# Kernel tuning notes

Hardware: AMD Instinct MI355X
Metric: run time of the kernel (lower is better)

The kernel has to match this reference:

```python
import jax, jax.numpy as jnp
import numpy as np
from jax import lax

P = 10  # patch_size


def _conv(x, w, b, pad):
    y = lax.conv_general_dilated(x, w, (1, 1), [(pad, pad), (pad, pad)],
                                 dimension_numbers=('NCHW', 'OIHW', 'NCHW'))
    return y + b[None, :, None, None]


def setup_inputs() -> dict:
    key = jax.random.key(0)
    ks = jax.random.split(key, 9)
    B, Cin, H, W = 8, 3, 320, 320
    classes = 2
    p2 = P * P
    s = 0.05
    return {
        'x': jax.random.normal(ks[0], (B, Cin, H, W), jnp.float32),
        'w_conv1': jax.random.normal(ks[1], (64, Cin, 7, 7), jnp.float32) * s,
        'b_conv1': jax.random.normal(ks[2], (64,), jnp.float32) * s,
        'w_conv2': jax.random.normal(ks[3], (classes, 64, 3, 3), jnp.float32) * s,
        'b_conv2': jax.random.normal(ks[4], (classes,), jnp.float32) * s,
        'w_fm': jax.random.normal(ks[5], (classes, Cin, 1, 1), jnp.float32) * s,
        'b_fm': jax.random.normal(ks[6], (classes,), jnp.float32) * s,
        'w_lin1': jax.random.normal(ks[7], (2 * p2, p2), jnp.float32) * s,  # torch Linear [out,in]
        'w_lin2': jax.random.normal(ks[8], (p2, 2 * p2), jnp.float32) * s,
    }


def reference(x, w_conv1, b_conv1, w_conv2, b_conv2, w_fm, b_fm, w_lin1, w_lin2):
    p = P
    ini = _conv(_conv(x, w_conv1, b_conv1, 3), w_conv2, b_conv2, 1)  # [B,classes,H,W]
    fea = _conv(x, w_fm, b_fm, 0) / 4.0                              # [B,classes,H,W]
    B, C, H, W = ini.shape
    L = (H // p) * (W // p)

    def unfold(t):  # non-overlapping patches: [B,C,H,W] -> [B,C,L,p*p]
        t = t.reshape(B, C, H // p, p, W // p, p)
        return t.transpose(0, 1, 2, 4, 3, 5).reshape(B, C, L, p * p)

    def trans(t):  # Linear(p2->2p2) -> Linear(2p2->p2) -> ReLU, per patch
        h = jnp.einsum('bclp,qp->bclq', t, w_lin1)
        return jax.nn.relu(jnp.einsum('bclq,pq->bclp', h, w_lin2))

    ui = trans(unfold(ini))   # [B,C,L,p2]
    uf = trans(unfold(fea))   # [B,C,L,p2]
    att = jnp.einsum('bclp,bcmp->bclm', ui, uf) / (p * p)  # [B,C,L,L]
    return att
```

## Files before the change

### kernel.cpp

```cpp
#include <hip/hip_runtime.h>

#define WS_M      0
#define WS_K      10000
#define WS_BETA   12646
#define WS_W9     12664
#define WS_BT     13150
#define WS_UIT    (16384 + 1638400)
#define WS_UFT    (16384 + 2*1638400)

typedef short bf16x8 __attribute__((ext_vector_type(8)));
typedef float f32x4  __attribute__((ext_vector_type(4)));

__device__ inline ushort f2bf(float f) {
    unsigned u = __float_as_uint(f);
    unsigned r = (u + 0x7fffu + ((u >> 16) & 1u)) >> 16;
    return (ushort)r;
}

__global__ __launch_bounds__(256) void k_prep(const float* __restrict__ wl1,
                                              const float* __restrict__ wl2,
                                              const float* __restrict__ wc1,
                                              const float* __restrict__ bc1,
                                              const float* __restrict__ wc2,
                                              const float* __restrict__ bc2,
                                              float* __restrict__ ws) {
    int blk = blockIdx.x;
    int t = threadIdx.x;
    if (blk < 40) {
        int idx = blk * 256 + t;
        if (idx < 10000) {
            int p = idx / 100, r = idx % 100;
            float s = 0.f;
            for (int q = 0; q < 200; ++q)
                s += wl2[p * 200 + q] * wl1[q * 100 + r];
            ws[WS_M + r * 100 + p] = s;
        }
        return;
    }
    __shared__ float swc1[9408];
    __shared__ float swc2[1152];
    __shared__ float sBeta[18];
    for (int i = t; i < 9408; i += 256) swc1[i] = wc1[i];
    for (int i = t; i < 1152; i += 256) swc2[i] = wc2[i];
    __syncthreads();
    if (blk < 43) {
        int base = (blk - 40) * 882;
        for (int ii = t; ii < 882; ii += 256) {
            int idx = base + ii;
            int v = idx % 7; int t1 = idx / 7;
            int u = t1 % 7;  int t2 = t1 / 7;
            int ci = t2 % 3; int t3 = t2 / 3;
            int b = t3 % 3;  int t4 = t3 / 3;
            int a = t4 % 3;  int c = t4 / 3;
            float s = 0.f;
            for (int c64 = 0; c64 < 64; ++c64)
                s += swc2[((c * 64 + c64) * 3 + a) * 3 + b] *
                     swc1[((c64 * 3 + ci) * 7 + u) * 7 + v];
            ws[WS_K + idx] = s;
        }
        if (blk == 40) {
            if (t < 18) {
                int b = t % 3; int a = (t / 3) % 3; int c = t / 9;
                float s = 0.f;
                for (int c64 = 0; c64 < 64; ++c64)
                    s += swc2[((c * 64 + c64) * 3 + a) * 3 + b] * bc1[c64];
                sBeta[t] = s; ws[WS_BETA + t] = s;
            }
            __syncthreads();
            if (t < 2) {
                float s = bc2[t];
                for (int j2 = 0; j2 < 9; ++j2) s += sBeta[t * 9 + j2];
                ws[WS_BT + t] = s;
            }
        }
    } else {
        int idx = (blk - 43) * 243 + t;
        if (t < 243) {
            int dx = idx % 9; int t1 = idx / 9;
            int dy = t1 % 9;  int t2 = t1 / 9;
            int ci = t2 % 3;  int c = t2 / 3;
            float s = 0.f;
            for (int a = 0; a < 3; ++a) {
                int u = dy - a; if (u < 0 || u > 6) continue;
                for (int b = 0; b < 3; ++b) {
                    int v = dx - b; if (v < 0 || v > 6) continue;
                    for (int c64 = 0; c64 < 64; ++c64)
                        s += swc2[((c * 64 + c64) * 3 + a) * 3 + b] *
                             swc1[((c64 * 3 + ci) * 7 + u) * 7 + v];
                }
            }
            ws[WS_W9 + idx] = s;
        }
    }
}

__global__ __launch_bounds__(256, 8) void k_fuse(const float* __restrict__ x,
                                                 const float* __restrict__ wfm,
                                                 const float* __restrict__ bfm,
                                                 const float* __restrict__ ws,
                                                 ushort* __restrict__ uiL,
                                                 ushort* __restrict__ ufL) {
    union alignas(16) SMemU {
        float  sx[3][28][36];
        ushort sOut[2][2][4][128];
    };
    __shared__ SMemU smu;
    __shared__ float sP[2][2][100][4];
    const int bx = blockIdx.x, by = blockIdx.y, b = blockIdx.z;
    const int t = threadIdx.x;
    const float* Mt   = ws + WS_M;
    const float* Kw   = ws + WS_K;
    const float* Beta = ws + WS_BETA;
    const float* W9   = ws + WS_W9;
    const float* Bt   = ws + WS_BT;
    const int gh0 = by * 20, gw0 = bx * 20;
    bool edgeblk = (by == 0) | (by == 15) | (bx == 0) | (bx == 15);

    if (!edgeblk) {
        for (int i = t; i < 588; i += 256) {
            int ci = i / 196; int rem = i - ci * 196;
            int rr = rem / 7, c4 = rem - rr * 7;
            float4 v = *(const float4*)&x[(b * 3 + ci) * 102400 +
                                          (gh0 - 4 + rr) * 320 + (gw0 - 4) + c4 * 4];
            *(float4*)&smu.sx[ci][rr][c4 * 4] = v;
        }
    } else {
        for (int idx = t; idx < 3 * 28 * 28; idx += 256) {
            int ci = idx / 784; int rem = idx - ci * 784;
            int rr = rem / 28, cc = rem - rr * 28;
            int gh = gh0 - 4 + rr, gw = gw0 - 4 + cc;
            float v = 0.f;
            if ((unsigned)gh < 320u && (unsigned)gw < 320u)
                v = x[(b * 3 + ci) * 102400 + gh * 320 + gw];
            smu.sx[ci][rr][cc] = v;
        }
    }
    __syncthreads();

    const int lh = t / 10, lw0 = (t % 10) * 2;
    if (t < 200) {
        float acc0[2], acc1[2];
        float bt0 = Bt[0], bt1 = Bt[1];
        acc0[0] = bt0; acc0[1] = bt0; acc1[0] = bt1; acc1[1] = bt1;
        #pragma unroll
        for (int ci = 0; ci < 3; ++ci) {
            #pragma unroll
            for (int dy = 0; dy < 9; ++dy) {
                const float* xr = &smu.sx[ci][lh + dy][lw0];
                float2 y0 = *(const float2*)(xr);
                float2 y1 = *(const float2*)(xr + 2);
                float2 y2 = *(const float2*)(xr + 4);
                float2 y3 = *(const float2*)(xr + 6);
                float2 y4 = *(const float2*)(xr + 8);
                float xv[10] = {y0.x, y0.y, y1.x, y1.y, y2.x,
                                y2.y, y3.x, y3.y, y4.x, y4.y};
                #pragma unroll
                for (int dx = 0; dx < 9; ++dx) {
                    float w0t = W9[ci * 81 + dy * 9 + dx];
                    float w1t = W9[243 + ci * 81 + dy * 9 + dx];
                    acc0[0] += w0t * xv[dx];
                    acc0[1] += w0t * xv[dx + 1];
                    acc1[0] += w1t * xv[dx];
                    acc1[1] += w1t * xv[dx + 1];
                }
            }
        }
        if (edgeblk) {
            #pragma unroll
            for (int j = 0; j < 2; ++j) {
                int h = gh0 + lh, w = gw0 + lw0 + j;
                if (h == 0 || h == 319 || w == 0 || w == 319) {
                    float c0 = 0.f, c1 = 0.f;
                    for (int a = 0; a < 3; ++a) {
                        int hh = h + a - 1;
                        for (int bb = 0; bb < 3; ++bb) {
                            int wwp = w + bb - 1;
                            bool invalid = ((unsigned)hh >= 320u) |
                                           ((unsigned)wwp >= 320u);
                            if (invalid) {
                                c0 += Beta[a * 3 + bb];
                                c1 += Beta[9 + a * 3 + bb];
                                for (int ci = 0; ci < 3; ++ci) {
                                    const float* Kc = Kw + ((a * 3 + bb) * 3 + ci) * 49;
                                    #pragma unroll
                                    for (int u = 0; u < 7; ++u) {
                                        #pragma unroll
                                        for (int v = 0; v < 7; ++v) {
                                            float xv = smu.sx[ci][lh + a + u][lw0 + j + bb + v];
                                            c0 += Kc[u * 7 + v] * xv;
                                            c1 += Kc[1323 + u * 7 + v] * xv;
                                        }
                                    }
                                }
                            }
                        }
                    }
                    acc0[j] -= c0;
                    acc1[j] -= c1;
                }
            }
        }
        float wf00 = wfm[0], wf01 = wfm[1], wf02 = wfm[2];
        float wf10 = wfm[3], wf11 = wfm[4], wf12 = wfm[5];
        float bf0 = bfm[0], bf1 = bfm[1];
        #pragma unroll
        for (int j = 0; j < 2; ++j) {
            int lw = lw0 + j;
            int li = (lh / 10) * 2 + lw / 10;
            int r  = (lh % 10) * 10 + lw % 10;
            sP[0][0][r][li] = acc0[j];
            sP[0][1][r][li] = acc1[j];
            float s0 = smu.sx[0][4 + lh][4 + lw];
            float s1 = smu.sx[1][4 + lh][4 + lw];
            float s2 = smu.sx[2][4 + lh][4 + lw];
            sP[1][0][r][li] = (bf0 + s0 * wf00 + s1 * wf01 + s2 * wf02) * 0.25f;
            sP[1][1][r][li] = (bf1 + s0 * wf10 + s1 * wf11 + s2 * wf12) * 0.25f;
        }
    }
    __syncthreads();

    if (t < 200) {
        int plane = (t >= 100) ? 1 : 0;
        int p = t - plane * 100;
        float ai[4] = {0.f, 0.f, 0.f, 0.f};
        float af[4] = {0.f, 0.f, 0.f, 0.f};
        #pragma unroll 4
        for (int r = 0; r < 100; ++r) {
            float m = Mt[r * 100 + p];
            f32x4 si = *(const f32x4*)&sP[0][plane][r][0];
            f32x4 sf = *(const f32x4*)&sP[1][plane][r][0];
            #pragma unroll
            for (int k = 0; k < 4; ++k) {
                ai[k] += m * si[k];
                af[k] += m * sf[k];
            }
        }
        #pragma unroll
        for (int k = 0; k < 4; ++k) {
            smu.sOut[0][plane][k][p] = f2bf(fmaxf(ai[k], 0.f));
            smu.sOut[1][plane][k][p] = f2bf(fmaxf(af[k], 0.f));
        }
    } else {
        #pragma unroll
        for (int pass = 0; pass < 2; ++pass) {
            int task = (t - 200) + pass * 56;
            int mat = task / 56; int rem = task % 56;
            int plane = rem / 28; int rem2 = rem % 28;
            int k = rem2 / 7, q = rem2 % 7;
            *(uint2*)&smu.sOut[mat][plane][k][100 + q * 4] = make_uint2(0u, 0u);
        }
    }
    __syncthreads();

    {
        int mat = t >> 7;
        int row = (t >> 4) & 7;
        int plane = row >> 2, k = row & 3;
        int lane16 = t & 15;
        int bc = b * 2 + plane;
        int l = (by * 2 + (k >> 1)) * 32 + bx * 2 + (k & 1);
        ushort* dst = mat ? ufL : uiL;
        uint4 v = *(const uint4*)&smu.sOut[mat][plane][k][lane16 * 8];
        *(uint4*)&dst[((size_t)bc * 1024 + l) * 128 + lane16 * 8] = v;
    }
}

__global__ __launch_bounds__(256) void k_att(const ushort* __restrict__ ui,
                                             const ushort* __restrict__ uf,
                                             float* __restrict__ out) {
    int bc   = blockIdx.z;
    int row0 = blockIdx.y * 64, col0 = blockIdx.x * 128;
    int wave = threadIdx.x >> 6, lane = threadIdx.x & 63;
    int r0 = row0 + (wave >> 1) * 32;
    int c0 = col0 + (wave & 1) * 64;
    int m = lane & 15, quad = lane >> 4;
    const ushort* ub = ui + (size_t)bc * 1024 * 128;
    const ushort* vb = uf + (size_t)bc * 1024 * 128;
    f32x4 acc[2][4];
    #pragma unroll
    for (int i = 0; i < 2; ++i)
        #pragma unroll
        for (int j = 0; j < 4; ++j)
            acc[i][j] = (f32x4){0.f, 0.f, 0.f, 0.f};
    #pragma unroll
    for (int k0 = 0; k0 < 128; k0 += 32) {
        bf16x8 af[2], bfr[4];
        #pragma unroll
        for (int i = 0; i < 2; ++i)
            af[i] = *(const bf16x8*)&ub[(size_t)(r0 + i * 16 + m) * 128 + k0 + quad * 8];
        #pragma unroll
        for (int j = 0; j < 4; ++j)
            bfr[j] = *(const bf16x8*)&vb[(size_t)(c0 + j * 16 + m) * 128 + k0 + quad * 8];
        #pragma unroll
        for (int i = 0; i < 2; ++i)
            #pragma unroll
            for (int j = 0; j < 4; ++j)
                acc[i][j] = __builtin_amdgcn_mfma_f32_16x16x32_bf16(af[i], bfr[j], acc[i][j], 0, 0, 0);
    }
    #pragma unroll
    for (int i = 0; i < 2; ++i) {
        #pragma unroll
        for (int r = 0; r < 4; ++r) {
            int row = r0 + i * 16 + quad * 4 + r;
            float* o = out + ((size_t)bc * 1024 + row) * 1024;
            #pragma unroll
            for (int j = 0; j < 4; ++j)
                o[c0 + j * 16 + m] = acc[i][j][r] * 0.01f;
        }
    }
}

extern "C" void kernel_launch(void* const* d_in, const int* in_sizes, int n_in,
                              void* d_out, int out_size, void* d_ws, size_t ws_size,
                              hipStream_t stream) {
    const float* x       = (const float*)d_in[0];
    const float* w_conv1 = (const float*)d_in[1];
    const float* b_conv1 = (const float*)d_in[2];
    const float* w_conv2 = (const float*)d_in[3];
    const float* b_conv2 = (const float*)d_in[4];
    const float* w_fm    = (const float*)d_in[5];
    const float* b_fm    = (const float*)d_in[6];
    const float* w_lin1  = (const float*)d_in[7];
    const float* w_lin2  = (const float*)d_in[8];
    float* out = (float*)d_out;
    float* ws  = (float*)d_ws;
    ushort* uiL = (ushort*)(ws + WS_UIT);
    ushort* ufL = (ushort*)(ws + WS_UFT);

    k_prep<<<45, 256, 0, stream>>>(w_lin1, w_lin2, w_conv1, b_conv1, w_conv2, b_conv2, ws);
    k_fuse<<<dim3(16, 16, 8), 256, 0, stream>>>(x, w_fm, b_fm, ws, uiL, ufL);
    k_att<<<dim3(8, 16, 16), 256, 0, stream>>>(uiL, ufL, out);
}
```

Before: 201.3 us.

## Split fused conv+patch-transform kernel into separate conv and transform kernels

```diff
diff --git a/kernel.cpp b/kernel.cpp
--- a/kernel.cpp
+++ b/kernel.cpp
@@ -5,6 +5,7 @@
 #define WS_BETA   12646
 #define WS_W9     12664
 #define WS_BT     13150
+#define WS_INI    16384
 #define WS_UIT    (16384 + 1638400)
 #define WS_UFT    (16384 + 2*1638400)
 
@@ -94,21 +95,12 @@
     }
 }
 
-__global__ __launch_bounds__(256, 8) void k_fuse(const float* __restrict__ x,
-                                                 const float* __restrict__ wfm,
-                                                 const float* __restrict__ bfm,
+__global__ __launch_bounds__(256, 8) void k_conv(const float* __restrict__ x,
                                                  const float* __restrict__ ws,
-                                                 ushort* __restrict__ uiL,
-                                                 ushort* __restrict__ ufL) {
-    union alignas(16) SMemU {
-        float  sx[3][28][36];
-        ushort sOut[2][2][4][128];
-    };
-    __shared__ SMemU smu;
-    __shared__ float sP[2][2][100][4];
+                                                 float* __restrict__ ini) {
+    __shared__ float sx[3][28][36];
     const int bx = blockIdx.x, by = blockIdx.y, b = blockIdx.z;
     const int t = threadIdx.x;
-    const float* Mt   = ws + WS_M;
     const float* Kw   = ws + WS_K;
     const float* Beta = ws + WS_BETA;
     const float* W9   = ws + WS_W9;
@@ -122,7 +114,7 @@
             int rr = rem / 7, c4 = rem - rr * 7;
             float4 v = *(const float4*)&x[(b * 3 + ci) * 102400 +
                                           (gh0 - 4 + rr) * 320 + (gw0 - 4) + c4 * 4];
-            *(float4*)&smu.sx[ci][rr][c4 * 4] = v;
+            *(float4*)&sx[ci][rr][c4 * 4] = v;
         }
     } else {
         for (int idx = t; idx < 3 * 28 * 28; idx += 256) {
@@ -132,7 +124,7 @@
             float v = 0.f;
             if ((unsigned)gh < 320u && (unsigned)gw < 320u)
                 v = x[(b * 3 + ci) * 102400 + gh * 320 + gw];
-            smu.sx[ci][rr][cc] = v;
+            sx[ci][rr][cc] = v;
         }
     }
     __syncthreads();
@@ -146,7 +138,7 @@
         for (int ci = 0; ci < 3; ++ci) {
             #pragma unroll
             for (int dy = 0; dy < 9; ++dy) {
-                const float* xr = &smu.sx[ci][lh + dy][lw0];
+                const float* xr = &sx[ci][lh + dy][lw0];
                 float2 y0 = *(const float2*)(xr);
                 float2 y1 = *(const float2*)(xr + 2);
                 float2 y2 = *(const float2*)(xr + 4);
@@ -186,7 +178,7 @@
                                     for (int u = 0; u < 7; ++u) {
                                         #pragma unroll
                                         for (int v = 0; v < 7; ++v) {
-                                            float xv = smu.sx[ci][lh + a + u][lw0 + j + bb + v];
+                                            float xv = sx[ci][lh + a + u][lw0 + j + bb + v];
                                             c0 += Kc[u * 7 + v] * xv;
                                             c1 += Kc[1323 + u * 7 + v] * xv;
                                         }
@@ -200,68 +192,106 @@
                 }
             }
         }
-        float wf00 = wfm[0], wf01 = wfm[1], wf02 = wfm[2];
-        float wf10 = wfm[3], wf11 = wfm[4], wf12 = wfm[5];
-        float bf0 = bfm[0], bf1 = bfm[1];
-        #pragma unroll
-        for (int j = 0; j < 2; ++j) {
-            int lw = lw0 + j;
-            int li = (lh / 10) * 2 + lw / 10;
-            int r  = (lh % 10) * 10 + lw % 10;
-            sP[0][0][r][li] = acc0[j];
-            sP[0][1][r][li] = acc1[j];
-            float s0 = smu.sx[0][4 + lh][4 + lw];
-            float s1 = smu.sx[1][4 + lh][4 + lw];
-            float s2 = smu.sx[2][4 + lh][4 + lw];
-            sP[1][0][r][li] = (bf0 + s0 * wf00 + s1 * wf01 + s2 * wf02) * 0.25f;
-            sP[1][1][r][li] = (bf1 + s0 * wf10 + s1 * wf11 + s2 * wf12) * 0.25f;
+        size_t obase = (size_t)(b * 2) * 102400 + (gh0 + lh) * 320 + gw0 + lw0;
+        *(float2*)&ini[obase] = make_float2(acc0[0], acc0[1]);
+        *(float2*)&ini[obase + 102400] = make_float2(acc1[0], acc1[1]);
+    }
+}
+
+__global__ __launch_bounds__(256) void k_trans(const float* __restrict__ ini,
+                                               const float* __restrict__ x,
+                                               const float* __restrict__ wfm,
+                                               const float* __restrict__ bfm,
+                                               const float* __restrict__ ws,
+                                               ushort* __restrict__ uiL,
+                                               ushort* __restrict__ ufL) {
+    __shared__ float  sP[100][68];
+    __shared__ ushort sOut[64][64];
+    int bc = blockIdx.x;
+    int lg = blockIdx.y;
+    int zz = blockIdx.z;
+    int mode = zz >> 1, pg = zz & 1;
+    ushort* outL = mode ? ufL : uiL;
+    int t = threadIdx.x;
+    const float* Mt = ws + WS_M;
+    int b = bc >> 1, c = bc & 1;
+    int row0 = lg * 20;
+
+    if (mode == 0) {
+        for (int e = t; e < 1600; e += 256) {
+            int irow = e / 80, c4 = (e % 80) * 4;
+            float4 v = *(const float4*)&ini[bc * 102400 + (row0 + irow) * 320 + c4];
+            float vv[4] = {v.x, v.y, v.z, v.w};
+            #pragma unroll
+            for (int k = 0; k < 4; ++k) {
+                int col = c4 + k;
+                sP[(irow % 10) * 10 + col % 10][(irow / 10) * 32 + col / 10] = vv[k];
+            }
+        }
+    } else {
+        float wf0 = wfm[c * 3 + 0], wf1 = wfm[c * 3 + 1], wf2 = wfm[c * 3 + 2];
+        float bfv = bfm[c];
+        for (int e = t; e < 1600; e += 256) {
+            int irow = e / 80, c4 = (e % 80) * 4;
+            size_t base = (size_t)b * 3 * 102400 + (row0 + irow) * 320 + c4;
+            float4 v0 = *(const float4*)&x[base];
+            float4 v1 = *(const float4*)&x[base + 102400];
+            float4 v2 = *(const float4*)&x[base + 204800];
+            float a0[4] = {v0.x, v0.y, v0.z, v0.w};
+            float a1[4] = {v1.x, v1.y, v1.z, v1.w};
+            float a2[4] = {v2.x, v2.y, v2.z, v2.w};
+            #pragma unroll
+            for (int k = 0; k < 4; ++k) {
+                int col = c4 + k;
+                float val = (bfv + a0[k] * wf0 + a1[k] * wf1 + a2[k] * wf2) * 0.25f;
+                sP[(irow % 10) * 10 + col % 10][(irow / 10) * 32 + col / 10] = val;
+            }
         }
     }
     __syncthreads();
 
     if (t < 200) {
-        int plane = (t >= 100) ? 1 : 0;
-        int p = t - plane * 100;
-        float ai[4] = {0.f, 0.f, 0.f, 0.f};
-        float af[4] = {0.f, 0.f, 0.f, 0.f};
-        #pragma unroll 4
+        int py = t / 8, lx = t % 8;
+        int p0 = py * 2, lo = lx * 8;
+        float acc[2][8];
+        #pragma unroll
+        for (int i = 0; i < 2; ++i)
+            #pragma unroll
+            for (int j = 0; j < 8; ++j) acc[i][j] = 0.f;
+        #pragma unroll 5
         for (int r = 0; r < 100; ++r) {
-            float m = Mt[r * 100 + p];
-            f32x4 si = *(const f32x4*)&sP[0][plane][r][0];
-            f32x4 sf = *(const f32x4*)&sP[1][plane][r][0];
-            #pragma unroll
-            for (int k = 0; k < 4; ++k) {
-                ai[k] += m * si[k];
-                af[k] += m * sf[k];
-            }
-        }
-        #pragma unroll
-        for (int k = 0; k < 4; ++k) {
-            smu.sOut[0][plane][k][p] = f2bf(fmaxf(ai[k], 0.f));
-            smu.sOut[1][plane][k][p] = f2bf(fmaxf(af[k], 0.f));
+            float2 mv = *(const float2*)&Mt[r * 100 + pg * 50 + p0];
+            f32x4 b0 = *(const f32x4*)&sP[r][lo];
+            f32x4 b1 = *(const f32x4*)&sP[r][lo + 4];
+            #pragma unroll
+            for (int j = 0; j < 4; ++j) {
+                acc[0][j]     += mv.x * b0[j];
+                acc[0][4 + j] += mv.x * b1[j];
+                acc[1][j]     += mv.y * b0[j];
+                acc[1][4 + j] += mv.y * b1[j];
+            }
+        }
+        #pragma unroll
+        for (int j = 0; j < 8; ++j) {
+            unsigned v0 = f2bf(fmaxf(acc[0][j], 0.f));
+            unsigned v1 = f2bf(fmaxf(acc[1][j], 0.f));
+            *(unsigned*)&sOut[lo + j][p0] = v0 | (v1 << 16);
         }
     } else {
         #pragma unroll
-        for (int pass = 0; pass < 2; ++pass) {
-            int task = (t - 200) + pass * 56;
-            int mat = task / 56; int rem = task % 56;
-            int plane = rem / 28; int rem2 = rem % 28;
-            int k = rem2 / 7, q = rem2 % 7;
-            *(uint2*)&smu.sOut[mat][plane][k][100 + q * 4] = make_uint2(0u, 0u);
+        for (int k = 0; k < 8; ++k) {
+            int idx = (t - 200) + 56 * k;
+            int l = idx / 7, q = idx % 7;
+            *(unsigned*)&sOut[l][50 + q * 2] = 0u;
         }
     }
     __syncthreads();
 
     {
-        int mat = t >> 7;
-        int row = (t >> 4) & 7;
-        int plane = row >> 2, k = row & 3;
-        int lane16 = t & 15;
-        int bc = b * 2 + plane;
-        int l = (by * 2 + (k >> 1)) * 32 + bx * 2 + (k & 1);
-        ushort* dst = mat ? ufL : uiL;
-        uint4 v = *(const uint4*)&smu.sOut[mat][plane][k][lane16 * 8];
-        *(uint4*)&dst[((size_t)bc * 1024 + l) * 128 + lane16 * 8] = v;
+        int l = t >> 2, q = t & 3;
+        size_t rowb = ((size_t)bc * 1024 + lg * 64 + l) * 128 + pg * 64;
+        *(uint4*)&outL[rowb + q * 8]      = *(const uint4*)&sOut[l][q * 8];
+        *(uint4*)&outL[rowb + 32 + q * 8] = *(const uint4*)&sOut[l][32 + q * 8];
     }
 }
 
@@ -328,6 +358,7 @@
     ushort* ufL = (ushort*)(ws + WS_UFT);
 
     k_prep<<<45, 256, 0, stream>>>(w_lin1, w_lin2, w_conv1, b_conv1, w_conv2, b_conv2, ws);
-    k_fuse<<<dim3(16, 16, 8), 256, 0, stream>>>(x, w_fm, b_fm, ws, uiL, ufL);
+    k_conv<<<dim3(16, 16, 8), 256, 0, stream>>>(x, ws, ws + WS_INI);
+    k_trans<<<dim3(16, 16, 4), 256, 0, stream>>>(ws + WS_INI, x, w_fm, b_fm, ws, uiL, ufL);
     k_att<<<dim3(8, 16, 16), 256, 0, stream>>>(uiL, ufL, out);
 }
```

Measured after the change: 208.3 us. 3.5% more time.
